# Kernel optimization log

Measured on AMD Instinct MI355X. Metric: run time of the kernel, lower is better.

Reference implementation:

```python
import jax, jax.numpy as jnp
import numpy as np

INPUT_DIM, QK_DIM, V_DIM = 1024, 512, 512

def setup_inputs() -> dict:
    key = jax.random.key(0)
    ks = jax.random.split(key, 7)
    B, S = 4, 2048
    scale = 1.0 / np.sqrt(INPUT_DIM)
    return {
        "x": jax.random.normal(ks[0], (B, S, INPUT_DIM), dtype=jnp.float32),
        "Wq": jax.random.normal(ks[1], (INPUT_DIM, QK_DIM), dtype=jnp.float32) * scale,
        "bq": jax.random.normal(ks[2], (QK_DIM,), dtype=jnp.float32) * 0.01,
        "Wk": jax.random.normal(ks[3], (INPUT_DIM, QK_DIM), dtype=jnp.float32) * scale,
        "bk": jax.random.normal(ks[4], (QK_DIM,), dtype=jnp.float32) * 0.01,
        "Wv": jax.random.normal(ks[5], (INPUT_DIM, V_DIM), dtype=jnp.float32) * scale,
        "bv": jax.random.normal(ks[6], (V_DIM,), dtype=jnp.float32) * 0.01,
    }

def reference(x, Wq, bq, Wk, bk, Wv, bv):
    # q,k: (B,S,Dqk), v: (B,S,Dv)
    q = jnp.einsum("bsi,id->bsd", x, Wq) + bq
    k = jnp.einsum("bsi,id->bsd", x, Wk) + bk
    v = jnp.einsum("bsi,id->bsd", x, Wv) + bv
    scale = 1.0 / jnp.sqrt(jnp.asarray(q.shape[-1], q.dtype))
    scores = jnp.einsum("bqd,bkd->bqk", q, k) * scale  # (B,S,S)
    attn = jax.nn.softmax(scores, axis=-1)
    return jnp.einsum("bqk,bkd->bqd", attn, v)
```

## Files before the change

kernel.cpp:

```cpp
#include <hip/hip_runtime.h>

typedef __attribute__((ext_vector_type(8))) short short8;
typedef __attribute__((ext_vector_type(4))) float f32x4;

#define S_    2048
#define DI    1024
#define DQK   512
#define DV    512
#define NTOK  8192

#define GLL(gp, lp) __builtin_amdgcn_global_load_lds( \
    (const __attribute__((address_space(1))) unsigned int*)(gp), \
    (__attribute__((address_space(3))) unsigned int*)(lp), 16, 0, 0)

static __device__ __forceinline__ unsigned short f2bf(float f) {
  unsigned int u = __float_as_uint(f);
  u += 0x7fffu + ((u >> 16) & 1u);
  return (unsigned short)(u >> 16);
}

__global__ void conv_x_kernel(const float* __restrict__ x,
                              unsigned short* __restrict__ xb, int n) {
  int idx = (blockIdx.x * 256 + threadIdx.x) * 8;
  if (idx >= n) return;
  const float4* p = (const float4*)(x + idx);
  float4 f0 = p[0], f1 = p[1];
  uint4 o;
  o.x = (unsigned)f2bf(f0.x) | ((unsigned)f2bf(f0.y) << 16);
  o.y = (unsigned)f2bf(f0.z) | ((unsigned)f2bf(f0.w) << 16);
  o.z = (unsigned)f2bf(f1.x) | ((unsigned)f2bf(f1.y) << 16);
  o.w = (unsigned)f2bf(f1.z) | ((unsigned)f2bf(f1.w) << 16);
  *(uint4*)(xb + idx) = o;
}

__global__ void conv_wT_kernel(const float* __restrict__ W0, const float* __restrict__ W1,
                               const float* __restrict__ W2,
                               unsigned short* __restrict__ T0, unsigned short* __restrict__ T1,
                               unsigned short* __restrict__ T2,
                               float* __restrict__ rowsum) {
  __shared__ float tile[32][33];
  int mat = blockIdx.z;
  if (mat == 0 && blockIdx.x == 0)
    rowsum[blockIdx.y * 256 + threadIdx.x] = 0.f;
  const float* W = (mat == 0) ? W0 : (mat == 1) ? W1 : W2;
  unsigned short* T = (mat == 0) ? T0 : (mat == 1) ? T1 : T2;
  int n0 = blockIdx.x * 32, k0 = blockIdx.y * 32;
  int c = threadIdx.x & 31, r0 = threadIdx.x >> 5;
  for (int i = 0; i < 4; ++i) {
    int kk = r0 + i * 8;
    tile[kk][c] = W[(k0 + kk) * DQK + n0 + c];
  }
  __syncthreads();
  for (int i = 0; i < 4; ++i) {
    int nn = r0 + i * 8;
    T[(n0 + nn) * DI + k0 + c] = f2bf(tile[c][nn]);
  }
}

__device__ __forceinline__ void gemm_core_dbuf(
    const unsigned short* __restrict__ A, const unsigned short* __restrict__ B,
    int lda, int ldb, int K, int m0, int n0,
    unsigned short (*As)[128 * 32], unsigned short (*Bs)[128 * 32],
    f32x4 (&acc)[4][4]) {
  int tid = threadIdx.x, lane = tid & 63, wv = tid >> 6;
  int quad = lane >> 4, l16 = lane & 15;
  int wm = wv >> 1, wn = wv & 1;
  int srow = tid >> 2;
  int sc = (tid & 3) ^ (srow & 3);
  const unsigned short* gA0 = A + (size_t)(m0 + srow) * lda + sc * 8;
  const unsigned short* gA1 = A + (size_t)(m0 + 64 + srow) * lda + sc * 8;
  const unsigned short* gB0 = B + (size_t)(n0 + srow) * ldb + sc * 8;
  const unsigned short* gB1 = B + (size_t)(n0 + 64 + srow) * ldb + sc * 8;
  int d0 = wv * 512;
  int d1 = 2048 + wv * 512;
#pragma unroll
  for (int i = 0; i < 4; ++i)
#pragma unroll
    for (int j = 0; j < 4; ++j) acc[i][j] = (f32x4){0.f, 0.f, 0.f, 0.f};

  auto stage = [&](int buf, int k0) {
    GLL(gA0 + k0, &As[buf][d0]);
    GLL(gA1 + k0, &As[buf][d1]);
    GLL(gB0 + k0, &Bs[buf][d0]);
    GLL(gB1 + k0, &Bs[buf][d1]);
  };

  int pc = (quad ^ (l16 & 3)) * 8;
  int nk = K >> 5;
  stage(0, 0);
  for (int kt = 0; kt < nk; ++kt) {
    int cur = kt & 1;
    __syncthreads();
    if (kt + 1 < nk) stage(cur ^ 1, (kt + 1) * 32);
    short8 af[4], bf[4];
#pragma unroll
    for (int t = 0; t < 4; ++t) {
      af[t] = *(const short8*)(&As[cur][(wm * 64 + t * 16 + l16) * 32 + pc]);
      bf[t] = *(const short8*)(&Bs[cur][(wn * 64 + t * 16 + l16) * 32 + pc]);
    }
#pragma unroll
    for (int tm = 0; tm < 4; ++tm)
#pragma unroll
      for (int tn = 0; tn < 4; ++tn)
        acc[tm][tn] = __builtin_amdgcn_mfma_f32_16x16x32_bf16(af[tm], bf[tn], acc[tm][tn], 0, 0, 0);
  }
}

__global__ __launch_bounds__(256, 3) void qkv_dma_kernel(
    const unsigned short* __restrict__ xb,
    const unsigned short* __restrict__ wqt, const unsigned short* __restrict__ wkt,
    const unsigned short* __restrict__ wvt,
    const float* __restrict__ bq, const float* __restrict__ bk, const float* __restrict__ bv,
    unsigned short* __restrict__ qo, unsigned short* __restrict__ ko,
    unsigned short* __restrict__ vto) {
  __shared__ unsigned short As[2][128 * 32];
  __shared__ unsigned short Bs[2][128 * 32];
  int bidx = blockIdx.x;
  int xcd = bidx & 7;
  int local = bidx >> 3;
  int mlocal = local & 7;
  int col12 = local >> 3;
  int mat = col12 >> 2;
  int m0 = (xcd * 8 + mlocal) * 128;
  int n0 = (col12 & 3) * 128;
  const unsigned short* wt = (mat == 0) ? wqt : (mat == 1) ? wkt : wvt;
  const float* bias = (mat == 0) ? bq : (mat == 1) ? bk : bv;
  float oscale = (mat == 0) ? 0.04419417382415922f : 1.0f;
  f32x4 acc[4][4];
  gemm_core_dbuf(xb, wt, DI, DI, DI, m0, n0, As, Bs, acc);

  int tid = threadIdx.x, lane = tid & 63, wv = tid >> 6;
  int quad = lane >> 4, l16 = lane & 15;
  int wm = wv >> 1, wn = wv & 1;
  bool transp = (mat == 2);
  unsigned short* outp = (mat == 0) ? qo : (mat == 1) ? ko : vto;
#pragma unroll
  for (int tn = 0; tn < 4; ++tn) {
    int col = n0 + wn * 64 + tn * 16 + l16;
    float bc = bias[col];
#pragma unroll
    for (int tm = 0; tm < 4; ++tm) {
      int rowb = m0 + wm * 64 + tm * 16 + quad * 4;
      f32x4 a = acc[tm][tn];
      if (!transp) {
        outp[(size_t)(rowb + 0) * DQK + col] = f2bf((a.x + bc) * oscale);
        outp[(size_t)(rowb + 1) * DQK + col] = f2bf((a.y + bc) * oscale);
        outp[(size_t)(rowb + 2) * DQK + col] = f2bf((a.z + bc) * oscale);
        outp[(size_t)(rowb + 3) * DQK + col] = f2bf((a.w + bc) * oscale);
      } else {
        ushort4 pk;
        pk.x = f2bf(a.x + bc); pk.y = f2bf(a.y + bc);
        pk.z = f2bf(a.z + bc); pk.w = f2bf(a.w + bc);
        *(ushort4*)(outp + (size_t)col * NTOK + rowb) = pk;
      }
    }
  }
}

__global__ __launch_bounds__(256, 4) void s_exp_kernel(
    const unsigned short* __restrict__ q, const unsigned short* __restrict__ k,
    unsigned short* __restrict__ sp, float* __restrict__ rowsum) {
  __shared__ unsigned short As[2][128 * 32];
  __shared__ unsigned short Bs[2][128 * 32];
  int bidx = blockIdx.x;
  int xcd = bidx & 7, b = xcd >> 1;
  int sub = ((bidx >> 3) << 1) | (xcd & 1);
  int m0 = (sub >> 4) * 128, n0 = (sub & 15) * 128;
  f32x4 acc[4][4];
  gemm_core_dbuf(q + (size_t)b * S_ * DQK, k + (size_t)b * S_ * DQK,
                 DQK, DQK, DQK, m0, n0, As, Bs, acc);

  int tid = threadIdx.x, lane = tid & 63, wv = tid >> 6;
  int quad = lane >> 4, l16 = lane & 15;
  int wm = wv >> 1, wn = wv & 1;
  unsigned short* Cb = sp + (size_t)b * S_ * S_;
#pragma unroll
  for (int tm = 0; tm < 4; ++tm) {
    int rowb = m0 + wm * 64 + tm * 16 + quad * 4;
    float rs[4] = {0.f, 0.f, 0.f, 0.f};
#pragma unroll
    for (int tn = 0; tn < 4; ++tn) {
      int col = n0 + wn * 64 + tn * 16 + l16;
      f32x4 a = acc[tm][tn];
      float e0 = __expf(a.x), e1 = __expf(a.y), e2 = __expf(a.z), e3 = __expf(a.w);
      Cb[(size_t)(rowb + 0) * S_ + col] = f2bf(e0);
      Cb[(size_t)(rowb + 1) * S_ + col] = f2bf(e1);
      Cb[(size_t)(rowb + 2) * S_ + col] = f2bf(e2);
      Cb[(size_t)(rowb + 3) * S_ + col] = f2bf(e3);
      rs[0] += e0; rs[1] += e1; rs[2] += e2; rs[3] += e3;
    }
    for (int off = 1; off < 16; off <<= 1)
#pragma unroll
      for (int r = 0; r < 4; ++r) rs[r] += __shfl_xor(rs[r], off);
    if (l16 == 0)
#pragma unroll
      for (int r = 0; r < 4; ++r) atomicAdd(rowsum + b * S_ + rowb + r, rs[r]);
  }
}

__global__ __launch_bounds__(256, 4) void pv_kernel(
    const unsigned short* __restrict__ sp, const unsigned short* __restrict__ vt,
    const float* __restrict__ rowsum, float* __restrict__ out) {
  __shared__ unsigned short As[2][64 * 64];
  __shared__ unsigned short Bs[2][64 * 64];
  int bidx = blockIdx.x;
  int xcd = bidx & 7, b = xcd >> 1;
  int sub = ((bidx >> 3) << 1) | (xcd & 1);
  int m0 = (sub >> 3) * 64, n0 = (sub & 7) * 64;
  int tid = threadIdx.x, lane = tid & 63, wv = tid >> 6;
  int quad = lane >> 4, l16 = lane & 15;
  int wm = wv >> 1, wn = wv & 1;
  const unsigned short* A = sp + (size_t)b * S_ * S_;
  const unsigned short* B = vt + (size_t)b * S_;

  int srow = tid >> 3;
  int schunk = (tid & 7) ^ (srow & 7);
  const unsigned short* gA0 = A + (size_t)(m0 + srow) * S_ + schunk * 8;
  const unsigned short* gA1 = A + (size_t)(m0 + 32 + srow) * S_ + schunk * 8;
  const unsigned short* gB0 = B + (size_t)(n0 + srow) * NTOK + schunk * 8;
  const unsigned short* gB1 = B + (size_t)(n0 + 32 + srow) * NTOK + schunk * 8;
  int ldsw0 = (wv * 8) * 64;
  int ldsw1 = (32 + wv * 8) * 64;

  f32x4 acc[2][2];
#pragma unroll
  for (int i = 0; i < 2; ++i)
#pragma unroll
    for (int j = 0; j < 2; ++j) acc[i][j] = (f32x4){0.f, 0.f, 0.f, 0.f};

  auto stage = [&](int buf, int k0) {
    GLL(gA0 + k0, &As[buf][ldsw0]);
    GLL(gA1 + k0, &As[buf][ldsw1]);
    GLL(gB0 + k0, &Bs[buf][ldsw0]);
    GLL(gB1 + k0, &Bs[buf][ldsw1]);
  };

  stage(0, 0);
  for (int kt = 0; kt < 32; ++kt) {
    int cur = kt & 1;
    __syncthreads();
    if (kt + 1 < 32) stage(cur ^ 1, (kt + 1) * 64);
#pragma unroll
    for (int ks = 0; ks < 2; ++ks) {
      int pc = ((ks * 4 + quad) ^ (l16 & 7)) * 8;
      short8 af[2], bf[2];
#pragma unroll
      for (int t = 0; t < 2; ++t) {
        af[t] = *(const short8*)(&As[cur][(wm * 32 + t * 16 + l16) * 64 + pc]);
        bf[t] = *(const short8*)(&Bs[cur][(wn * 32 + t * 16 + l16) * 64 + pc]);
      }
#pragma unroll
      for (int tm = 0; tm < 2; ++tm)
#pragma unroll
        for (int tn = 0; tn < 2; ++tn)
          acc[tm][tn] = __builtin_amdgcn_mfma_f32_16x16x32_bf16(af[tm], bf[tn], acc[tm][tn], 0, 0, 0);
    }
  }

  float* ob = out + (size_t)b * S_ * DV;
#pragma unroll
  for (int tm = 0; tm < 2; ++tm) {
    int rowb = m0 + wm * 32 + tm * 16 + quad * 4;
    float inv[4];
#pragma unroll
    for (int i = 0; i < 4; ++i) inv[i] = 1.0f / rowsum[b * S_ + rowb + i];
#pragma unroll
    for (int tn = 0; tn < 2; ++tn) {
      int col = n0 + wn * 32 + tn * 16 + l16;
      f32x4 a = acc[tm][tn];
      ob[(size_t)(rowb + 0) * DV + col] = a.x * inv[0];
      ob[(size_t)(rowb + 1) * DV + col] = a.y * inv[1];
      ob[(size_t)(rowb + 2) * DV + col] = a.z * inv[2];
      ob[(size_t)(rowb + 3) * DV + col] = a.w * inv[3];
    }
  }
}

extern "C" void kernel_launch(void* const* d_in, const int* in_sizes, int n_in,
                              void* d_out, int out_size, void* d_ws, size_t ws_size,
                              hipStream_t stream) {
  const float* x  = (const float*)d_in[0];
  const float* Wq = (const float*)d_in[1];
  const float* bq = (const float*)d_in[2];
  const float* Wk = (const float*)d_in[3];
  const float* bk = (const float*)d_in[4];
  const float* Wv = (const float*)d_in[5];
  const float* bv = (const float*)d_in[6];
  float* out = (float*)d_out;

  char* ws = (char*)d_ws;
  unsigned short* xb  = (unsigned short*)(ws);
  unsigned short* wqt = (unsigned short*)(ws + 16777216);
  unsigned short* wkt = (unsigned short*)(ws + 16777216 + 1048576);
  unsigned short* wvt = (unsigned short*)(ws + 16777216 + 2097152);
  unsigned short* qo  = (unsigned short*)(ws + 19922944);
  unsigned short* ko  = (unsigned short*)(ws + 19922944 + 8388608);
  unsigned short* vto = (unsigned short*)(ws + 19922944 + 16777216);
  unsigned short* sp  = (unsigned short*)(ws + 45088768);
  float* rowsum       = (float*)(ws + 45088768 + 33554432);

  conv_x_kernel<<<4096, 256, 0, stream>>>(x, xb, NTOK * DI);
  dim3 gw(16, 32, 3);
  conv_wT_kernel<<<gw, 256, 0, stream>>>(Wq, Wk, Wv, wqt, wkt, wvt, rowsum);
  qkv_dma_kernel<<<768, 256, 0, stream>>>(xb, wqt, wkt, wvt, bq, bk, bv, qo, ko, vto);
  s_exp_kernel<<<1024, 256, 0, stream>>>(qo, ko, sp, rowsum);
  pv_kernel<<<1024, 256, 0, stream>>>(sp, vto, rowsum, out);
}
```

Before: 183.9 us.

## Stage GEMM epilogues through LDS for coalesced 16-byte stores; merge prep kernels

The epilogues of the QKV, S=exp(QK^T) and PV kernels now write their output tiles into shared memory, which reuses the GEMM staging buffers with a padded stride. After a barrier, each thread copies contiguous 16-byte chunks to global memory. The old epilogues issued scattered 2-byte bf16 or 4-byte float stores per element. The x conversion and the weight-transpose kernels are also merged into one launch to save a kernel launch. In exchange, the epilogues gain extra barriers and an LDS round trip, and the QKV and S kernels use more shared memory, which may reduce occupancy.

New measurement: 188.3 us. +2.4%, slower.

```diff
diff --git a/kernel.cpp b/kernel.cpp
--- a/kernel.cpp
+++ b/kernel.cpp
@@ -8,6 +8,7 @@
 #define DQK   512
 #define DV    512
 #define NTOK  8192
+#define CSTR  136
 
 #define GLL(gp, lp) __builtin_amdgcn_global_load_lds( \
     (const __attribute__((address_space(1))) unsigned int*)(gp), \
@@ -19,32 +20,33 @@
   return (unsigned short)(u >> 16);
 }
 
-__global__ void conv_x_kernel(const float* __restrict__ x,
-                              unsigned short* __restrict__ xb, int n) {
-  int idx = (blockIdx.x * 256 + threadIdx.x) * 8;
-  if (idx >= n) return;
-  const float4* p = (const float4*)(x + idx);
-  float4 f0 = p[0], f1 = p[1];
-  uint4 o;
-  o.x = (unsigned)f2bf(f0.x) | ((unsigned)f2bf(f0.y) << 16);
-  o.y = (unsigned)f2bf(f0.z) | ((unsigned)f2bf(f0.w) << 16);
-  o.z = (unsigned)f2bf(f1.x) | ((unsigned)f2bf(f1.y) << 16);
-  o.w = (unsigned)f2bf(f1.z) | ((unsigned)f2bf(f1.w) << 16);
-  *(uint4*)(xb + idx) = o;
-}
-
-__global__ void conv_wT_kernel(const float* __restrict__ W0, const float* __restrict__ W1,
-                               const float* __restrict__ W2,
-                               unsigned short* __restrict__ T0, unsigned short* __restrict__ T1,
-                               unsigned short* __restrict__ T2,
-                               float* __restrict__ rowsum) {
+__global__ void prep_kernel(const float* __restrict__ x, unsigned short* __restrict__ xb,
+                            const float* __restrict__ W0, const float* __restrict__ W1,
+                            const float* __restrict__ W2,
+                            unsigned short* __restrict__ T0, unsigned short* __restrict__ T1,
+                            unsigned short* __restrict__ T2,
+                            float* __restrict__ rowsum) {
   __shared__ float tile[32][33];
-  int mat = blockIdx.z;
-  if (mat == 0 && blockIdx.x == 0)
-    rowsum[blockIdx.y * 256 + threadIdx.x] = 0.f;
+  int bid = blockIdx.x;
+  if (bid < 4096) {
+    int idx = (bid * 256 + threadIdx.x) * 8;
+    const float4* p = (const float4*)(x + idx);
+    float4 f0 = p[0], f1 = p[1];
+    uint4 o;
+    o.x = (unsigned)f2bf(f0.x) | ((unsigned)f2bf(f0.y) << 16);
+    o.y = (unsigned)f2bf(f0.z) | ((unsigned)f2bf(f0.w) << 16);
+    o.z = (unsigned)f2bf(f1.x) | ((unsigned)f2bf(f1.y) << 16);
+    o.w = (unsigned)f2bf(f1.z) | ((unsigned)f2bf(f1.w) << 16);
+    *(uint4*)(xb + idx) = o;
+    return;
+  }
+  int b2 = bid - 4096;
+  int mat = b2 >> 9;
+  int rem = b2 & 511;
+  if (mat == 0 && rem < 32) rowsum[rem * 256 + threadIdx.x] = 0.f;
   const float* W = (mat == 0) ? W0 : (mat == 1) ? W1 : W2;
   unsigned short* T = (mat == 0) ? T0 : (mat == 1) ? T1 : T2;
-  int n0 = blockIdx.x * 32, k0 = blockIdx.y * 32;
+  int n0 = (rem & 15) * 32, k0 = (rem >> 4) * 32;
   int c = threadIdx.x & 31, r0 = threadIdx.x >> 5;
   for (int i = 0; i < 4; ++i) {
     int kk = r0 + i * 8;
@@ -113,8 +115,9 @@
     const float* __restrict__ bq, const float* __restrict__ bk, const float* __restrict__ bv,
     unsigned short* __restrict__ qo, unsigned short* __restrict__ ko,
     unsigned short* __restrict__ vto) {
-  __shared__ unsigned short As[2][128 * 32];
-  __shared__ unsigned short Bs[2][128 * 32];
+  __shared__ unsigned short smem[128 * CSTR];
+  unsigned short (*As)[4096] = (unsigned short (*)[4096])smem;
+  unsigned short (*Bs)[4096] = (unsigned short (*)[4096])(smem + 8192);
   int bidx = blockIdx.x;
   int xcd = bidx & 7;
   int local = bidx >> 3;
@@ -133,35 +136,54 @@
   int quad = lane >> 4, l16 = lane & 15;
   int wm = wv >> 1, wn = wv & 1;
   bool transp = (mat == 2);
-  unsigned short* outp = (mat == 0) ? qo : (mat == 1) ? ko : vto;
+  __syncthreads();
 #pragma unroll
   for (int tn = 0; tn < 4; ++tn) {
-    int col = n0 + wn * 64 + tn * 16 + l16;
-    float bc = bias[col];
+    int cl = wn * 64 + tn * 16 + l16;
+    float bc = bias[n0 + cl];
 #pragma unroll
     for (int tm = 0; tm < 4; ++tm) {
-      int rowb = m0 + wm * 64 + tm * 16 + quad * 4;
+      int rl = wm * 64 + tm * 16 + quad * 4;
       f32x4 a = acc[tm][tn];
+      unsigned short v0 = f2bf((a.x + bc) * oscale);
+      unsigned short v1 = f2bf((a.y + bc) * oscale);
+      unsigned short v2 = f2bf((a.z + bc) * oscale);
+      unsigned short v3 = f2bf((a.w + bc) * oscale);
       if (!transp) {
-        outp[(size_t)(rowb + 0) * DQK + col] = f2bf((a.x + bc) * oscale);
-        outp[(size_t)(rowb + 1) * DQK + col] = f2bf((a.y + bc) * oscale);
-        outp[(size_t)(rowb + 2) * DQK + col] = f2bf((a.z + bc) * oscale);
-        outp[(size_t)(rowb + 3) * DQK + col] = f2bf((a.w + bc) * oscale);
+        smem[(rl + 0) * CSTR + cl] = v0;
+        smem[(rl + 1) * CSTR + cl] = v1;
+        smem[(rl + 2) * CSTR + cl] = v2;
+        smem[(rl + 3) * CSTR + cl] = v3;
       } else {
-        ushort4 pk;
-        pk.x = f2bf(a.x + bc); pk.y = f2bf(a.y + bc);
-        pk.z = f2bf(a.z + bc); pk.w = f2bf(a.w + bc);
-        *(ushort4*)(outp + (size_t)col * NTOK + rowb) = pk;
+        smem[cl * CSTR + rl + 0] = v0;
+        smem[cl * CSTR + rl + 1] = v1;
+        smem[cl * CSTR + rl + 2] = v2;
+        smem[cl * CSTR + rl + 3] = v3;
       }
     }
+  }
+  __syncthreads();
+  int r = tid >> 1, half = (tid & 1) * 64;
+  if (!transp) {
+    unsigned short* outp = (mat == 0) ? qo : ko;
+    unsigned short* gp = outp + (size_t)(m0 + r) * DQK + n0 + half;
+#pragma unroll
+    for (int j = 0; j < 8; ++j)
+      *(uint4*)(gp + j * 8) = *(const uint4*)(smem + r * CSTR + half + j * 8);
+  } else {
+    unsigned short* gp = vto + (size_t)(n0 + r) * NTOK + m0 + half;
+#pragma unroll
+    for (int j = 0; j < 8; ++j)
+      *(uint4*)(gp + j * 8) = *(const uint4*)(smem + r * CSTR + half + j * 8);
   }
 }
 
 __global__ __launch_bounds__(256, 4) void s_exp_kernel(
     const unsigned short* __restrict__ q, const unsigned short* __restrict__ k,
     unsigned short* __restrict__ sp, float* __restrict__ rowsum) {
-  __shared__ unsigned short As[2][128 * 32];
-  __shared__ unsigned short Bs[2][128 * 32];
+  __shared__ unsigned short smem[128 * CSTR];
+  unsigned short (*As)[4096] = (unsigned short (*)[4096])smem;
+  unsigned short (*Bs)[4096] = (unsigned short (*)[4096])(smem + 8192);
   int bidx = blockIdx.x;
   int xcd = bidx & 7, b = xcd >> 1;
   int sub = ((bidx >> 3) << 1) | (xcd & 1);
@@ -173,20 +195,20 @@
   int tid = threadIdx.x, lane = tid & 63, wv = tid >> 6;
   int quad = lane >> 4, l16 = lane & 15;
   int wm = wv >> 1, wn = wv & 1;
-  unsigned short* Cb = sp + (size_t)b * S_ * S_;
+  __syncthreads();
 #pragma unroll
   for (int tm = 0; tm < 4; ++tm) {
-    int rowb = m0 + wm * 64 + tm * 16 + quad * 4;
+    int rl = wm * 64 + tm * 16 + quad * 4;
     float rs[4] = {0.f, 0.f, 0.f, 0.f};
 #pragma unroll
     for (int tn = 0; tn < 4; ++tn) {
-      int col = n0 + wn * 64 + tn * 16 + l16;
+      int cl = wn * 64 + tn * 16 + l16;
       f32x4 a = acc[tm][tn];
       float e0 = __expf(a.x), e1 = __expf(a.y), e2 = __expf(a.z), e3 = __expf(a.w);
-      Cb[(size_t)(rowb + 0) * S_ + col] = f2bf(e0);
-      Cb[(size_t)(rowb + 1) * S_ + col] = f2bf(e1);
-      Cb[(size_t)(rowb + 2) * S_ + col] = f2bf(e2);
-      Cb[(size_t)(rowb + 3) * S_ + col] = f2bf(e3);
+      smem[(rl + 0) * CSTR + cl] = f2bf(e0);
+      smem[(rl + 1) * CSTR + cl] = f2bf(e1);
+      smem[(rl + 2) * CSTR + cl] = f2bf(e2);
+      smem[(rl + 3) * CSTR + cl] = f2bf(e3);
       rs[0] += e0; rs[1] += e1; rs[2] += e2; rs[3] += e3;
     }
     for (int off = 1; off < 16; off <<= 1)
@@ -194,15 +216,22 @@
       for (int r = 0; r < 4; ++r) rs[r] += __shfl_xor(rs[r], off);
     if (l16 == 0)
 #pragma unroll
-      for (int r = 0; r < 4; ++r) atomicAdd(rowsum + b * S_ + rowb + r, rs[r]);
-  }
+      for (int r = 0; r < 4; ++r) atomicAdd(rowsum + b * S_ + m0 + rl + r, rs[r]);
+  }
+  __syncthreads();
+  int r = tid >> 1, half = (tid & 1) * 64;
+  unsigned short* gp = sp + (size_t)b * S_ * S_ + (size_t)(m0 + r) * S_ + n0 + half;
+#pragma unroll
+  for (int j = 0; j < 8; ++j)
+    *(uint4*)(gp + j * 8) = *(const uint4*)(smem + r * CSTR + half + j * 8);
 }
 
 __global__ __launch_bounds__(256, 4) void pv_kernel(
     const unsigned short* __restrict__ sp, const unsigned short* __restrict__ vt,
     const float* __restrict__ rowsum, float* __restrict__ out) {
-  __shared__ unsigned short As[2][64 * 64];
-  __shared__ unsigned short Bs[2][64 * 64];
+  __shared__ unsigned short smem[16384];
+  unsigned short (*As)[4096] = (unsigned short (*)[4096])smem;
+  unsigned short (*Bs)[4096] = (unsigned short (*)[4096])(smem + 8192);
   int bidx = blockIdx.x;
   int xcd = bidx & 7, b = xcd >> 1;
   int sub = ((bidx >> 3) << 1) | (xcd & 1);
@@ -257,23 +286,30 @@
     }
   }
 
-  float* ob = out + (size_t)b * S_ * DV;
+  float* ct = (float*)smem;
+  __syncthreads();
 #pragma unroll
   for (int tm = 0; tm < 2; ++tm) {
-    int rowb = m0 + wm * 32 + tm * 16 + quad * 4;
+    int rl = wm * 32 + tm * 16 + quad * 4;
     float inv[4];
 #pragma unroll
-    for (int i = 0; i < 4; ++i) inv[i] = 1.0f / rowsum[b * S_ + rowb + i];
+    for (int i = 0; i < 4; ++i) inv[i] = 1.0f / rowsum[b * S_ + m0 + rl + i];
 #pragma unroll
     for (int tn = 0; tn < 2; ++tn) {
-      int col = n0 + wn * 32 + tn * 16 + l16;
+      int cl = wn * 32 + tn * 16 + l16;
       f32x4 a = acc[tm][tn];
-      ob[(size_t)(rowb + 0) * DV + col] = a.x * inv[0];
-      ob[(size_t)(rowb + 1) * DV + col] = a.y * inv[1];
-      ob[(size_t)(rowb + 2) * DV + col] = a.z * inv[2];
-      ob[(size_t)(rowb + 3) * DV + col] = a.w * inv[3];
-    }
-  }
+      ct[(rl + 0) * 68 + cl] = a.x * inv[0];
+      ct[(rl + 1) * 68 + cl] = a.y * inv[1];
+      ct[(rl + 2) * 68 + cl] = a.z * inv[2];
+      ct[(rl + 3) * 68 + cl] = a.w * inv[3];
+    }
+  }
+  __syncthreads();
+  int r = tid >> 2, qc = (tid & 3) * 16;
+  float* ob = out + (size_t)b * S_ * DV + (size_t)(m0 + r) * DV + n0 + qc;
+#pragma unroll
+  for (int j = 0; j < 4; ++j)
+    *(uint4*)(ob + j * 4) = *(const uint4*)(ct + r * 68 + qc + j * 4);
 }
 
 extern "C" void kernel_launch(void* const* d_in, const int* in_sizes, int n_in,
@@ -299,9 +335,7 @@
   unsigned short* sp  = (unsigned short*)(ws + 45088768);
   float* rowsum       = (float*)(ws + 45088768 + 33554432);
 
-  conv_x_kernel<<<4096, 256, 0, stream>>>(x, xb, NTOK * DI);
-  dim3 gw(16, 32, 3);
-  conv_wT_kernel<<<gw, 256, 0, stream>>>(Wq, Wk, Wv, wqt, wkt, wvt, rowsum);
+  prep_kernel<<<5632, 256, 0, stream>>>(x, xb, Wq, Wk, Wv, wqt, wkt, wvt, rowsum);
   qkv_dma_kernel<<<768, 256, 0, stream>>>(xb, wqt, wkt, wvt, bq, bk, bv, qo, ko, vto);
   s_exp_kernel<<<1024, 256, 0, stream>>>(qo, ko, sp, rowsum);
   pv_kernel<<<1024, 256, 0, stream>>>(sp, vto, rowsum, out);
```
